# Performance work log

Hardware: AMD Instinct MI355X
Metric: run time of the kernel (lower is better)

Reference implementation:

```python
import jax, jax.numpy as jnp
import numpy as np


def setup_inputs() -> dict:
    key = jax.random.key(0)
    x = jax.random.normal(key, (128, 256, 32, 32), dtype=jnp.float32)
    return {"x": x, "topk": 5}


def reference(x, topk):
    B = x.shape[0]
    flat = x.reshape(B, -1)                      # [B, N]
    _, idx = jax.lax.top_k(flat, topk)           # [B, k] indices into N
    out = jnp.zeros_like(flat)
    out = out.at[jnp.arange(B)[:, None], idx].set(1.0)
    return out.reshape(x.shape)
```

## Files before the change

### kernel.cpp

```cpp
#include <hip/hip_runtime.h>
#include <limits.h>
#include <math.h>

#define BROWS 128
#define NCOLS (256 * 32 * 32)
#define K 5
#define BPR 32
#define TPB 256
#define CHUNK (NCOLS / BPR)
#define F4_PER_THREAD (CHUNK / 4 / TPB)

__device__ __forceinline__ bool better(float av, int ai, float bv, int bi) {
    return (av > bv) || (av == bv && ai < bi);
}

__device__ __forceinline__ void insert5(float (&v)[K], int (&ix)[K], float cv, int ci) {
    if (better(cv, ci, v[K - 1], ix[K - 1])) {
        v[K - 1] = cv; ix[K - 1] = ci;
#pragma unroll
        for (int s = K - 1; s > 0; --s) {
            if (better(v[s], ix[s], v[s - 1], ix[s - 1])) {
                float tv = v[s]; v[s] = v[s - 1]; v[s - 1] = tv;
                int ti = ix[s]; ix[s] = ix[s - 1]; ix[s - 1] = ti;
            }
        }
    }
}

__device__ __forceinline__ void wave_reduce5(float (&v)[K], int (&ix)[K]) {
#pragma unroll
    for (int off = 1; off < 64; off <<= 1) {
        float ov[K]; int oi[K];
#pragma unroll
        for (int k = 0; k < K; ++k) {
            ov[k] = __shfl_xor(v[k], off, 64);
            oi[k] = __shfl_xor(ix[k], off, 64);
        }
#pragma unroll
        for (int k = 0; k < K; ++k) insert5(v, ix, ov[k], oi[k]);
    }
}

__global__ __launch_bounds__(TPB) void wta_scan(const float* __restrict__ x,
                                                float* __restrict__ out,
                                                float* __restrict__ wsv,
                                                int* __restrict__ wsi) {
    const int gb  = blockIdx.x;
    const int row = gb / BPR;
    const int blk = gb % BPR;
    const size_t base = (size_t)row * NCOLS + (size_t)blk * CHUNK;
    const float4* __restrict__ x4 = (const float4*)(x + base);
    float4* __restrict__ o4 = (float4*)(out + base);
    const int t = threadIdx.x;

    float4 r[F4_PER_THREAD];
#pragma unroll
    for (int i = 0; i < F4_PER_THREAD; ++i) r[i] = x4[t + i * TPB];

    const float4 z = make_float4(0.f, 0.f, 0.f, 0.f);
#pragma unroll
    for (int i = 0; i < F4_PER_THREAD; ++i) o4[t + i * TPB] = z;

    float v[K]; int ix[K];
#pragma unroll
    for (int k = 0; k < K; ++k) { v[k] = -INFINITY; ix[k] = INT_MAX; }

#pragma unroll
    for (int i = 0; i < F4_PER_THREAD; ++i) {
        const float4 d = r[i];
        const float m = fmaxf(fmaxf(d.x, d.y), fmaxf(d.z, d.w));
        if (m >= v[K - 1]) {
            const int e = blk * CHUNK + (t + i * TPB) * 4;
            insert5(v, ix, d.x, e + 0);
            insert5(v, ix, d.y, e + 1);
            insert5(v, ix, d.z, e + 2);
            insert5(v, ix, d.w, e + 3);
        }
    }

    wave_reduce5(v, ix);

    __shared__ float sv[TPB / 64][K];
    __shared__ int   si[TPB / 64][K];
    const int wave = t >> 6, lane = t & 63;
    if (lane == 0) {
#pragma unroll
        for (int k = 0; k < K; ++k) { sv[wave][k] = v[k]; si[wave][k] = ix[k]; }
    }
    __syncthreads();
    if (t == 0) {
#pragma unroll
        for (int w = 1; w < TPB / 64; ++w)
#pragma unroll
            for (int k = 0; k < K; ++k) insert5(v, ix, sv[w][k], si[w][k]);
        const int o = gb * K;
#pragma unroll
        for (int k = 0; k < K; ++k) { wsv[o + k] = v[k]; wsi[o + k] = ix[k]; }
    }
}

__global__ __launch_bounds__(64) void wta_final(const float* __restrict__ wsv,
                                                const int* __restrict__ wsi,
                                                float* __restrict__ out) {
    const int row  = blockIdx.x;
    const int lane = threadIdx.x;

    float v[K]; int ix[K];
#pragma unroll
    for (int k = 0; k < K; ++k) { v[k] = -INFINITY; ix[k] = INT_MAX; }

    const int ncand = BPR * K;
    for (int c = lane; c < ncand; c += 64)
        insert5(v, ix, wsv[row * ncand + c], wsi[row * ncand + c]);

    wave_reduce5(v, ix);

    if (lane == 0) {
#pragma unroll
        for (int k = 0; k < K; ++k)
            out[(size_t)row * NCOLS + ix[k]] = 1.0f;
    }
}

extern "C" void kernel_launch(void* const* d_in, const int* in_sizes, int n_in,
                              void* d_out, int out_size, void* d_ws, size_t ws_size,
                              hipStream_t stream) {
    const float* x = (const float*)d_in[0];
    float* out = (float*)d_out;
    float* wsv = (float*)d_ws;
    int*   wsi = (int*)((char*)d_ws + (size_t)BROWS * BPR * K * sizeof(float));

    wta_scan<<<BROWS * BPR, TPB, 0, stream>>>(x, out, wsv, wsi);
    wta_final<<<BROWS, 64, 0, stream>>>(wsv, wsi, out);
}
```

Before: 255.0 us.

## Software-pipeline scan loads, pack value/index into 64-bit keys, fewer blocks per row

Each row now uses 8 blocks instead of 32. Each thread streams its chunk in batches of 8 float4 loads, prefetching the next batch while it processes the current one, instead of loading the whole chunk into registers. The zero writes become nontemporal stores. Each value and index pair is packed into one order-preserving 64-bit key, so compares and shuffles work on a single key, and the final kernel reads 40 candidates with one load per lane. The batches are meant to overlap memory latency with compute and cut register pressure, at the cost of fewer blocks in flight per row.

Measured after the change: 261.9 us. 1.03x slower.

```diff
diff --git a/kernel.cpp b/kernel.cpp
--- a/kernel.cpp
+++ b/kernel.cpp
@@ -1,124 +1,147 @@
 #include <hip/hip_runtime.h>
 #include <limits.h>
 #include <math.h>
+#include <stdint.h>
 
 #define BROWS 128
 #define NCOLS (256 * 32 * 32)
 #define K 5
-#define BPR 32
+#define BPR 8
 #define TPB 256
 #define CHUNK (NCOLS / BPR)
-#define F4_PER_THREAD (CHUNK / 4 / TPB)
+#define F4T (CHUNK / 4 / TPB)
+#define BATCH 8
+#define NBATCH (F4T / BATCH)
 
-__device__ __forceinline__ bool better(float av, int ai, float bv, int bi) {
-    return (av > bv) || (av == bv && ai < bi);
+typedef float v4f __attribute__((ext_vector_type(4)));
+
+__device__ __forceinline__ uint64_t make_key(float f, uint32_t idx) {
+    uint32_t u = __float_as_uint(f);
+    u = (u & 0x80000000u) ? ~u : (u | 0x80000000u);
+    return ((uint64_t)u << 32) | (uint32_t)(~idx);
+}
+__device__ __forceinline__ float key_val(uint64_t k) {
+    uint32_t u = (uint32_t)(k >> 32);
+    u = (u & 0x80000000u) ? (u ^ 0x80000000u) : ~u;
+    return __uint_as_float(u);
+}
+__device__ __forceinline__ uint32_t key_idx(uint64_t k) {
+    return ~(uint32_t)k;
 }
 
-__device__ __forceinline__ void insert5(float (&v)[K], int (&ix)[K], float cv, int ci) {
-    if (better(cv, ci, v[K - 1], ix[K - 1])) {
-        v[K - 1] = cv; ix[K - 1] = ci;
+#define KEY_NEG_INF 0x007FFFFF00000000ULL
+
+__device__ __forceinline__ void insert5(uint64_t (&key)[K], uint64_t c) {
+    if (c > key[K - 1]) {
+        key[K - 1] = c;
 #pragma unroll
         for (int s = K - 1; s > 0; --s) {
-            if (better(v[s], ix[s], v[s - 1], ix[s - 1])) {
-                float tv = v[s]; v[s] = v[s - 1]; v[s - 1] = tv;
-                int ti = ix[s]; ix[s] = ix[s - 1]; ix[s - 1] = ti;
+            if (key[s] > key[s - 1]) {
+                uint64_t t = key[s]; key[s] = key[s - 1]; key[s - 1] = t;
             }
         }
     }
 }
 
-__device__ __forceinline__ void wave_reduce5(float (&v)[K], int (&ix)[K]) {
+__device__ __forceinline__ void wave_reduce5(uint64_t (&key)[K]) {
 #pragma unroll
     for (int off = 1; off < 64; off <<= 1) {
-        float ov[K]; int oi[K];
+        uint64_t ok[K];
 #pragma unroll
-        for (int k = 0; k < K; ++k) {
-            ov[k] = __shfl_xor(v[k], off, 64);
-            oi[k] = __shfl_xor(ix[k], off, 64);
-        }
+        for (int k = 0; k < K; ++k)
+            ok[k] = __shfl_xor((unsigned long long)key[k], off, 64);
 #pragma unroll
-        for (int k = 0; k < K; ++k) insert5(v, ix, ov[k], oi[k]);
+        for (int k = 0; k < K; ++k) insert5(key, ok[k]);
     }
 }
 
 __global__ __launch_bounds__(TPB) void wta_scan(const float* __restrict__ x,
                                                 float* __restrict__ out,
-                                                float* __restrict__ wsv,
-                                                int* __restrict__ wsi) {
+                                                uint64_t* __restrict__ wsk) {
     const int gb  = blockIdx.x;
     const int row = gb / BPR;
     const int blk = gb % BPR;
     const size_t base = (size_t)row * NCOLS + (size_t)blk * CHUNK;
     const float4* __restrict__ x4 = (const float4*)(x + base);
-    float4* __restrict__ o4 = (float4*)(out + base);
+    v4f* __restrict__ o4 = (v4f*)(out + base);
     const int t = threadIdx.x;
 
-    float4 r[F4_PER_THREAD];
+    uint64_t key[K];
 #pragma unroll
-    for (int i = 0; i < F4_PER_THREAD; ++i) r[i] = x4[t + i * TPB];
+    for (int k = 0; k < K; ++k) key[k] = KEY_NEG_INF;
+    float vmin = -INFINITY;
 
-    const float4 z = make_float4(0.f, 0.f, 0.f, 0.f);
+    const v4f z = {0.f, 0.f, 0.f, 0.f};
+
+    float4 cur[BATCH], nxt[BATCH];
 #pragma unroll
-    for (int i = 0; i < F4_PER_THREAD; ++i) o4[t + i * TPB] = z;
-
-    float v[K]; int ix[K];
-#pragma unroll
-    for (int k = 0; k < K; ++k) { v[k] = -INFINITY; ix[k] = INT_MAX; }
+    for (int j = 0; j < BATCH; ++j) cur[j] = x4[t + j * TPB];
 
 #pragma unroll
-    for (int i = 0; i < F4_PER_THREAD; ++i) {
-        const float4 d = r[i];
-        const float m = fmaxf(fmaxf(d.x, d.y), fmaxf(d.z, d.w));
-        if (m >= v[K - 1]) {
-            const int e = blk * CHUNK + (t + i * TPB) * 4;
-            insert5(v, ix, d.x, e + 0);
-            insert5(v, ix, d.y, e + 1);
-            insert5(v, ix, d.z, e + 2);
-            insert5(v, ix, d.w, e + 3);
+    for (int b = 0; b < NBATCH; ++b) {
+        if (b + 1 < NBATCH) {
+#pragma unroll
+            for (int j = 0; j < BATCH; ++j)
+                nxt[j] = x4[t + ((b + 1) * BATCH + j) * TPB];
         }
+#pragma unroll
+        for (int j = 0; j < BATCH; ++j)
+            __builtin_nontemporal_store(z, &o4[t + (b * BATCH + j) * TPB]);
+#pragma unroll
+        for (int j = 0; j < BATCH; ++j) {
+            const float4 d = cur[j];
+            const float m = fmaxf(fmaxf(d.x, d.y), fmaxf(d.z, d.w));
+            if (m >= vmin) {
+                const uint32_t e = (uint32_t)(blk * CHUNK) +
+                                   (uint32_t)(t + (b * BATCH + j) * TPB) * 4u;
+                insert5(key, make_key(d.x, e + 0));
+                insert5(key, make_key(d.y, e + 1));
+                insert5(key, make_key(d.z, e + 2));
+                insert5(key, make_key(d.w, e + 3));
+                vmin = key_val(key[K - 1]);
+            }
+        }
+#pragma unroll
+        for (int j = 0; j < BATCH; ++j) cur[j] = nxt[j];
     }
 
-    wave_reduce5(v, ix);
+    wave_reduce5(key);
 
-    __shared__ float sv[TPB / 64][K];
-    __shared__ int   si[TPB / 64][K];
+    __shared__ uint64_t sk[TPB / 64][K];
     const int wave = t >> 6, lane = t & 63;
     if (lane == 0) {
 #pragma unroll
-        for (int k = 0; k < K; ++k) { sv[wave][k] = v[k]; si[wave][k] = ix[k]; }
+        for (int k = 0; k < K; ++k) sk[wave][k] = key[k];
     }
     __syncthreads();
     if (t == 0) {
 #pragma unroll
         for (int w = 1; w < TPB / 64; ++w)
 #pragma unroll
-            for (int k = 0; k < K; ++k) insert5(v, ix, sv[w][k], si[w][k]);
-        const int o = gb * K;
+            for (int k = 0; k < K; ++k) insert5(key, sk[w][k]);
 #pragma unroll
-        for (int k = 0; k < K; ++k) { wsv[o + k] = v[k]; wsi[o + k] = ix[k]; }
+        for (int k = 0; k < K; ++k) wsk[gb * K + k] = key[k];
     }
 }
 
-__global__ __launch_bounds__(64) void wta_final(const float* __restrict__ wsv,
-                                                const int* __restrict__ wsi,
+__global__ __launch_bounds__(64) void wta_final(const uint64_t* __restrict__ wsk,
                                                 float* __restrict__ out) {
     const int row  = blockIdx.x;
     const int lane = threadIdx.x;
 
-    float v[K]; int ix[K];
+    uint64_t key[K];
 #pragma unroll
-    for (int k = 0; k < K; ++k) { v[k] = -INFINITY; ix[k] = INT_MAX; }
+    for (int k = 0; k < K; ++k) key[k] = KEY_NEG_INF;
 
     const int ncand = BPR * K;
-    for (int c = lane; c < ncand; c += 64)
-        insert5(v, ix, wsv[row * ncand + c], wsi[row * ncand + c]);
+    if (lane < ncand) insert5(key, wsk[row * ncand + lane]);
 
-    wave_reduce5(v, ix);
+    wave_reduce5(key);
 
     if (lane == 0) {
 #pragma unroll
         for (int k = 0; k < K; ++k)
-            out[(size_t)row * NCOLS + ix[k]] = 1.0f;
+            out[(size_t)row * NCOLS + key_idx(key[k])] = 1.0f;
     }
 }
 
@@ -127,9 +150,8 @@
                               hipStream_t stream) {
     const float* x = (const float*)d_in[0];
     float* out = (float*)d_out;
-    float* wsv = (float*)d_ws;
-    int*   wsi = (int*)((char*)d_ws + (size_t)BROWS * BPR * K * sizeof(float));
+    uint64_t* wsk = (uint64_t*)d_ws;
 
-    wta_scan<<<BROWS * BPR, TPB, 0, stream>>>(x, out, wsv, wsi);
-    wta_final<<<BROWS, 64, 0, stream>>>(wsv, wsi, out);
+    wta_scan<<<BROWS * BPR, TPB, 0, stream>>>(x, out, wsk);
+    wta_final<<<BROWS, 64, 0, stream>>>(wsk, out);
 }
```
